# Kernel optimization log

Measured on AMD Instinct MI355X. Metric: run time of the kernel, lower is better.

## Reference

```python
import jax, jax.numpy as jnp
import numpy as np
from jax import lax

GAMMA = 1.0
BIG = 1e8  # matches the torch init value 100000000.0


def setup_inputs() -> dict:
    key = jax.random.key(0)
    k1, k2 = jax.random.split(key)
    B, n, m, d = 256, 256, 256, 32
    x = jax.random.normal(k1, (B, n, d), dtype=jnp.float32)
    y = jax.random.normal(k2, (B, m, d), dtype=jnp.float32)
    return {"x": x, "y": y}


def _soft_dtw(x, y, gamma):
    B, n, d = x.shape
    m = y.shape[1]
    # squared euclidean distances, (B, n, m); GEMM form avoids the (B,n,m,d) blowup
    x2 = jnp.sum(x * x, axis=-1)
    y2 = jnp.sum(y * y, axis=-1)
    dist = x2[:, :, None] + y2[:, None, :] - 2.0 * jnp.einsum('bnd,bmd->bnm', x, y)
    dist = jnp.maximum(dist, 0.0)  # cdist(p=2)**2 is nonnegative

    def softmin3(a, b, c):
        s = jnp.stack([a, b, c], axis=0)
        return -gamma * jax.nn.logsumexp(-s / gamma, axis=0)

    big_col = jnp.full((B,), BIG, dtype=x.dtype)

    def row_step(prev_row, d_row):
        # prev_row: (B, m+1) = D[i-1, :];  d_row: (B, m) = dist[:, i-1, :]
        def col_step(cur, inp):
            # cur: (B,) = D[i, j-1]; inp: (dist[i-1,j-1], D[i-1,j], D[i-1,j-1])
            dij, up, diag = inp
            new = dij + softmin3(up, cur, diag)
            return new, new
        xs = (d_row.T, prev_row[:, 1:].T, prev_row[:, :-1].T)  # each (m, B)
        _, vals = lax.scan(col_step, big_col, xs)  # vals: (m, B)
        new_row = jnp.concatenate([big_col[:, None], vals.T], axis=1)  # (B, m+1)
        return new_row, None

    init_row = jnp.concatenate(
        [jnp.zeros((B, 1), x.dtype), jnp.full((B, m), BIG, dtype=x.dtype)], axis=1)
    final_row, _ = lax.scan(row_step, init_row, jnp.swapaxes(dist, 0, 1))  # scan over n rows
    return jnp.mean(final_row[:, m])


def reference(x, y):
    return _soft_dtw(x, y, GAMMA)
```

## Files before the change

kernel.cpp:

```cpp
#include <hip/hip_runtime.h>

#define BIG 1e8f
#define LN2 0.69314718f
#define LOG2E 1.44269504f
#define M2L -2.8853900818f

#define RSLOT 112
#define DRB 1040

#define OFF_XH   116480
#define OFF_X2S  132864
#define OFF_Y2S  133888
#define OFF_RDY  134912
#define OFF_PRG  134976
#define LDS_BYTES 135040

typedef _Float16 half8 __attribute__((ext_vector_type(8)));
typedef _Float16 half2_t __attribute__((ext_vector_type(2)));
typedef float f32x4 __attribute__((ext_vector_type(4)));

__device__ __forceinline__ float exp2g(float x) {
#if __has_builtin(__builtin_amdgcn_exp2f)
    return __builtin_amdgcn_exp2f(x);
#else
    return exp2f(x);
#endif
}
__device__ __forceinline__ float log2g(float x) {
#if __has_builtin(__builtin_amdgcn_logf)
    return __builtin_amdgcn_logf(x);
#else
    return log2f(x);
#endif
}

__device__ __forceinline__ half2_t pkrtz(float a, float b) {
    return __builtin_bit_cast(half2_t, __builtin_amdgcn_cvt_pkrtz(a, b));
}

__device__ __forceinline__ float shfl_up1(float v, float oldv) {
    int r = __builtin_amdgcn_update_dpp(
        __builtin_bit_cast(int, oldv), __builtin_bit_cast(int, v),
        0x138 , 0xf, 0xf, false);
    return __builtin_bit_cast(float, r);
}

__device__ __forceinline__ void dec2(unsigned int w, float& a, float& b) {
    half2_t h = __builtin_bit_cast(half2_t, w);
    a = (float)h[0];
    b = (float)h[1];
}

#define MASKW0 0x7BFF7BFFu
#define MASKW1 0x70007000u
#define MASKW2 0x60006000u
#define MASKW3 0x50005000u

__global__ __launch_bounds__(128, 1) void sdtw_kernel(
    const float* __restrict__ x, const float* __restrict__ y,
    float* __restrict__ out) {
    extern __shared__ __align__(16) char smem[];
    unsigned char* band = (unsigned char*)smem;
    _Float16* xh = (_Float16*)(smem + OFF_XH);
    float* x2sL = (float*)(smem + OFF_X2S);
    float* y2sL = (float*)(smem + OFF_Y2S);
    volatile int* rdy = (volatile int*)(smem + OFF_RDY);
    volatile int* prg = (volatile int*)(smem + OFF_PRG);

    const int tid = threadIdx.x;
    const int b = blockIdx.x;
    const float* xb = x + (size_t)b * 8192;
    const float* yb = y + (size_t)b * 8192;

#pragma unroll
    for (int rr = 0; rr < 2; rr++) {
        const int r = tid + rr * 128;
        const float4* px = (const float4*)(xb + r * 32);
        union { _Float16 h[32]; half8 v[4]; } uc;
        float s2 = 0.f;
#pragma unroll
        for (int q = 0; q < 8; q++) {
            float4 f = px[q];
            s2 += f.x * f.x + f.y * f.y + f.z * f.z + f.w * f.w;
            uc.h[4 * q + 0] = (_Float16)f.x;
            uc.h[4 * q + 1] = (_Float16)f.y;
            uc.h[4 * q + 2] = (_Float16)f.z;
            uc.h[4 * q + 3] = (_Float16)f.w;
        }
        half8* dst = (half8*)&xh[r * 32];
#pragma unroll
        for (int q = 0; q < 4; q++) dst[q] = uc.v[q];
        x2sL[r] = s2 * LOG2E;

        const float4* py = (const float4*)(yb + r * 32);
        float t2 = 0.f;
#pragma unroll
        for (int q = 0; q < 8; q++) {
            float4 f = py[q];
            t2 += f.x * f.x + f.y * f.y + f.z * f.z + f.w * f.w;
        }
        y2sL[r] = t2 * LOG2E;
    }
    if (tid < 16) rdy[tid] = 0;
    if (tid == 16) *prg = 0;
    __syncthreads();

    if (tid >= 64) {
        const int lane = tid - 64;
        const int qd = lane >> 4, xr = lane & 15;

        half8 yfrag[16];
        float yvL[16];
#pragma unroll
        for (int ci = 0; ci < 16; ci++) {
            const float* yp = yb + (ci * 16 + xr) * 32 + qd * 8;
            float4 f0 = *(const float4*)yp;
            float4 f1 = *(const float4*)(yp + 4);
            half8 v;
            v[0] = (_Float16)f0.x; v[1] = (_Float16)f0.y;
            v[2] = (_Float16)f0.z; v[3] = (_Float16)f0.w;
            v[4] = (_Float16)f1.x; v[5] = (_Float16)f1.y;
            v[6] = (_Float16)f1.z; v[7] = (_Float16)f1.w;
            yfrag[ci] = v;
            yvL[ci] = y2sL[ci * 16 + xr];
        }

        for (int sg = 0; sg < 16; sg++) {
            if (sg >= 6) {
                const int need = 8 * sg - 40;
                while (*prg < need) {}
            }
            const half8 xf = *(const half8*)&xh[(sg * 16 + xr) * 32 + qd * 8];
            const float4 xl = *(const float4*)&x2sL[sg * 16 + qd * 4];
            const int p0 = 8 * sg + 2 * qd;
#pragma unroll
            for (int ci = 0; ci < 16; ci++) {
                f32x4 acc = {0.f, 0.f, 0.f, 0.f};
                acc = __builtin_amdgcn_mfma_f32_16x16x32_f16(xf, yfrag[ci], acc, 0, 0, 0);
                const int c = ci * 16 + xr;
                const float yv = yvL[ci];
                const float d0 = fmaxf(fmaf(M2L, acc[0], xl.x + yv), 0.f);
                const float d1 = fmaxf(fmaf(M2L, acc[1], xl.y + yv), 0.f);
                const float d2 = fmaxf(fmaf(M2L, acc[2], xl.z + yv), 0.f);
                const float d3 = fmaxf(fmaf(M2L, acc[3], xl.w + yv), 0.f);
                const half2_t h01 = pkrtz(d0, d1);
                const half2_t h23 = pkrtz(d2, d3);
                const int dr0 = p0 + (c >> 2);
                int s0_ = dr0;     if (s0_ >= RSLOT) s0_ -= RSLOT;
                int s1_ = dr0 + 1; if (s1_ >= RSLOT) s1_ -= RSLOT;
                *(half2_t*)&band[s0_ * DRB + 4 * c] = h01;
                *(half2_t*)&band[s1_ * DRB + 4 * c] = h23;
            }
            __threadfence_block();
            if (lane == 0) rdy[sg] = 1;
        }
        return;
    }

    const int lane = tid;
    float MpA3 = BIG, SpA3 = 1.f, MpB3 = BIG, SpB3 = 1.f;
    float Mm[4], Sm[4];
    Mm[0] = (lane == 0) ? 0.f : BIG;
    Sm[0] = (lane == 0) ? 1.f : 2.f;
    Mm[1] = BIG; Sm[1] = 2.f;
    Mm[2] = BIG; Sm[2] = 2.f;
    Mm[3] = BIG; Sm[3] = 2.f;

    while (rdy[0] == 0) {}
    uint4 wreg = *(const uint4*)&band[16 * lane];

    auto step = [&](int s_) {
        const float MLA = shfl_up1(MpA3, BIG);
        const float MLB = shfl_up1(MpB3, BIG);
        const float SLA = shfl_up1(SpA3, 1.f);
        const float SLB = shfl_up1(SpB3, 1.f);

        const bool act = (unsigned)(s_ - lane - 1) < 128u;
        const unsigned wx = act ? wreg.x : MASKW0;
        const unsigned wy = act ? wreg.y : MASKW1;
        const unsigned wz = act ? wreg.z : MASKW2;
        const unsigned ww = act ? wreg.w : MASKW3;
        float dA[4], dB[4];
        dec2(wx, dA[0], dB[0]);
        dec2(wy, dA[1], dB[1]);
        dec2(wz, dA[2], dB[2]);
        dec2(ww, dA[3], dB[3]);

        int dn = (s_ > 190) ? 190 : s_;
        if (dn >= RSLOT) dn -= RSLOT;
        const uint4 wnext = *(const uint4*)&band[dn * DRB + 16 * lane];

        float MA[4], xAm[4], xAv[4];
        float prevA = MLA;
#pragma unroll
        for (int k = 0; k < 4; k++) {
            const float mu = fminf(Mm[k], prevA);
            xAm[k] = mu - Mm[k];
            xAv[k] = mu - prevA;
            MA[k] = dA[k] + mu;
            prevA = MA[k];
        }
        float muN[4], xNa[4], xNb[4];
        float diagA = MLA;
#pragma unroll
        for (int k = 0; k < 4; k++) {
            muN[k] = fminf(MA[k], diagA);
            xNa[k] = muN[k] - MA[k];
            xNb[k] = muN[k] - diagA;
            diagA = MA[k];
        }
        float MB[4], xBm[4], xBv[4];
        float prevB = MLB;
#pragma unroll
        for (int k = 0; k < 4; k++) {
            const float mu = fminf(muN[k], prevB);
            xBm[k] = mu - muN[k];
            xBv[k] = mu - prevB;
            MB[k] = dB[k] + mu;
            prevB = MB[k];
        }
        float muC[4], xCa[4], xCb[4];
        float diagB = MLB;
#pragma unroll
        for (int k = 0; k < 4; k++) {
            muC[k] = fminf(MB[k], diagB);
            xCa[k] = muC[k] - MB[k];
            xCb[k] = muC[k] - diagB;
            diagB = MB[k];
        }

        float eAm[4], eAv[4], eNa[4], eNb[4], eBm[4], eBv[4], eCa[4], eCb[4];
#pragma unroll
        for (int k = 0; k < 4; k++) {
            eAm[k] = exp2g(xAm[k]);
            eAv[k] = exp2g(xAv[k]);
            eNa[k] = exp2g(xNa[k]);
            eNb[k] = exp2g(xNb[k]);
            eBm[k] = exp2g(xBm[k]);
            eBv[k] = exp2g(xBv[k]);
            eCa[k] = exp2g(xCa[k]);
            eCb[k] = exp2g(xCb[k]);
        }

        float SA[4];
        float ps = SLA;
#pragma unroll
        for (int k = 0; k < 4; k++) {
            SA[k] = fmaf(Sm[k], eAm[k], ps * eAv[k]);
            ps = SA[k];
        }
        float SN[4];
        float dsg = SLA;
#pragma unroll
        for (int k = 0; k < 4; k++) {
            SN[k] = fmaf(SA[k], eNa[k], dsg * eNb[k]);
            dsg = SA[k];
        }
        float SB[4];
        ps = SLB;
#pragma unroll
        for (int k = 0; k < 4; k++) {
            SB[k] = fmaf(SN[k], eBm[k], ps * eBv[k]);
            ps = SB[k];
        }
        dsg = SLB;
#pragma unroll
        for (int k = 0; k < 4; k++) {
            Sm[k] = fmaf(SB[k], eCa[k], dsg * eCb[k]);
            dsg = SB[k];
        }

        MpA3 = MA[3]; SpA3 = SA[3];
        MpB3 = MB[3]; SpB3 = SB[3];
#pragma unroll
        for (int k = 0; k < 4; k++) Mm[k] = muC[k];
        wreg = wnext;
    };

#pragma unroll
    for (int s_ = 1; s_ < 8; s_++) step(s_);

    for (int g = 1; g < 24; g++) {
        int st = (g > 15) ? 15 : g;
        while (rdy[st] == 0) {}
        if (lane == 0) *prg = 8 * g;
        const int s0 = 8 * g;
#pragma unroll
        for (int k = 0; k < 8; k++) step(s0 + k);
    }

    if (lane == 63)
        atomicAdd(out, (MpB3 - log2g(SpB3)) * (LN2 / 256.f));
}

extern "C" void kernel_launch(void* const* d_in, const int* in_sizes, int n_in,
                              void* d_out, int out_size, void* d_ws, size_t ws_size,
                              hipStream_t stream) {
    const float* x = (const float*)d_in[0];
    const float* y = (const float*)d_in[1];
    float* out = (float*)d_out;
    const int B = in_sizes[0] / (256 * 32);

    (void)hipFuncSetAttribute((const void*)sdtw_kernel,
                              hipFuncAttributeMaxDynamicSharedMemorySize,
                              LDS_BYTES);
    (void)hipMemsetAsync(d_out, 0, sizeof(float), stream);
    sdtw_kernel<<<dim3(B), dim3(128), LDS_BYTES, stream>>>(x, y, out);
}
```

Baseline: 134.8 us.

## Split soft-DTW wavefront into max-track and sum-track warps pipelined through LDS

Splits the single recurrence wave into two: one wave tracks the running minimum (M) and writes the per-step exponent gaps to an 8-deep LDS ring, and a second wave consumes them to update the scaled sums (S). The exp2 work also drops from two calls per softmin pair to one, using a sign-select on the gap. The block grows to 192 threads with a third wave for distance MFMA. The band ring shrinks to make room for the gap buffer, and the producer lookahead is adjusted. This adds LDS traffic and spin-wait handshakes between waves in exchange for shortening the serial dependency chain on each wave.

New measurement: 130.3 us. 3.4% less time.

```diff
diff --git a/kernel.cpp b/kernel.cpp
--- a/kernel.cpp
+++ b/kernel.cpp
@@ -5,15 +5,20 @@
 #define LOG2E 1.44269504f
 #define M2L -2.8853900818f
 
-#define RSLOT 112
+#define RSLOT 104
 #define DRB 1040
 
-#define OFF_XH   116480
-#define OFF_X2S  132864
-#define OFF_Y2S  133888
-#define OFF_RDY  134912
-#define OFF_PRG  134976
-#define LDS_BYTES 135040
+#define OFF_XH    108160
+#define OFF_X2S   124544
+#define OFF_Y2S   125568
+#define OFF_DR    126592
+#define OFF_RDY   159360
+#define OFF_PRG   159424
+#define OFF_MPRG  159428
+#define OFF_SPRG  159432
+#define OFF_MDONE 159436
+#define OFF_MVAL  159440
+#define LDS_BYTES 159456
 
 typedef _Float16 half8 __attribute__((ext_vector_type(8)));
 typedef _Float16 half2_t __attribute__((ext_vector_type(2)));
@@ -56,7 +61,7 @@
 #define MASKW2 0x60006000u
 #define MASKW3 0x50005000u
 
-__global__ __launch_bounds__(128, 1) void sdtw_kernel(
+__global__ __launch_bounds__(192, 1) void sdtw_kernel(
     const float* __restrict__ x, const float* __restrict__ y,
     float* __restrict__ out) {
     extern __shared__ __align__(16) char smem[];
@@ -66,47 +71,56 @@
     float* y2sL = (float*)(smem + OFF_Y2S);
     volatile int* rdy = (volatile int*)(smem + OFF_RDY);
     volatile int* prg = (volatile int*)(smem + OFF_PRG);
+    volatile int* mprg = (volatile int*)(smem + OFF_MPRG);
+    volatile int* sprg = (volatile int*)(smem + OFF_SPRG);
+    volatile int* mdone = (volatile int*)(smem + OFF_MDONE);
+    volatile float* mval = (volatile float*)(smem + OFF_MVAL);
 
     const int tid = threadIdx.x;
     const int b = blockIdx.x;
     const float* xb = x + (size_t)b * 8192;
     const float* yb = y + (size_t)b * 8192;
 
-#pragma unroll
-    for (int rr = 0; rr < 2; rr++) {
-        const int r = tid + rr * 128;
-        const float4* px = (const float4*)(xb + r * 32);
-        union { _Float16 h[32]; half8 v[4]; } uc;
-        float s2 = 0.f;
-#pragma unroll
-        for (int q = 0; q < 8; q++) {
-            float4 f = px[q];
-            s2 += f.x * f.x + f.y * f.y + f.z * f.z + f.w * f.w;
-            uc.h[4 * q + 0] = (_Float16)f.x;
-            uc.h[4 * q + 1] = (_Float16)f.y;
-            uc.h[4 * q + 2] = (_Float16)f.z;
-            uc.h[4 * q + 3] = (_Float16)f.w;
-        }
-        half8* dst = (half8*)&xh[r * 32];
-#pragma unroll
-        for (int q = 0; q < 4; q++) dst[q] = uc.v[q];
-        x2sL[r] = s2 * LOG2E;
-
-        const float4* py = (const float4*)(yb + r * 32);
-        float t2 = 0.f;
-#pragma unroll
-        for (int q = 0; q < 8; q++) {
-            float4 f = py[q];
-            t2 += f.x * f.x + f.y * f.y + f.z * f.z + f.w * f.w;
-        }
-        y2sL[r] = t2 * LOG2E;
+    if (tid < 128) {
+#pragma unroll
+        for (int rr = 0; rr < 2; rr++) {
+            const int r = tid + rr * 128;
+            const float4* px = (const float4*)(xb + r * 32);
+            union { _Float16 h[32]; half8 v[4]; } uc;
+            float s2 = 0.f;
+#pragma unroll
+            for (int q = 0; q < 8; q++) {
+                float4 f = px[q];
+                s2 += f.x * f.x + f.y * f.y + f.z * f.z + f.w * f.w;
+                uc.h[4 * q + 0] = (_Float16)f.x;
+                uc.h[4 * q + 1] = (_Float16)f.y;
+                uc.h[4 * q + 2] = (_Float16)f.z;
+                uc.h[4 * q + 3] = (_Float16)f.w;
+            }
+            half8* dst = (half8*)&xh[r * 32];
+#pragma unroll
+            for (int q = 0; q < 4; q++) dst[q] = uc.v[q];
+            x2sL[r] = s2 * LOG2E;
+
+            const float4* py = (const float4*)(yb + r * 32);
+            float t2 = 0.f;
+#pragma unroll
+            for (int q = 0; q < 8; q++) {
+                float4 f = py[q];
+                t2 += f.x * f.x + f.y * f.y + f.z * f.z + f.w * f.w;
+            }
+            y2sL[r] = t2 * LOG2E;
+        }
     }
     if (tid < 16) rdy[tid] = 0;
     if (tid == 16) *prg = 0;
+    if (tid == 17) *mprg = 0;
+    if (tid == 18) *sprg = 0;
+    if (tid == 19) *mdone = 0;
     __syncthreads();
 
-    if (tid >= 64) {
-        const int lane = tid - 64;
+    if (tid >= 128) {
+        const int lane = tid - 128;
         const int qd = lane >> 4, xr = lane & 15;
 
         half8 yfrag[16];
@@ -126,8 +140,8 @@
         }
 
         for (int sg = 0; sg < 16; sg++) {
-            if (sg >= 6) {
-                const int need = 8 * sg - 40;
+            if (sg >= 5) {
+                const int need = 8 * sg - 32;
                 while (*prg < need) {}
             }
             const half8 xf = *(const half8*)&xh[(sg * 16 + xr) * 32 + qd * 8];
@@ -157,140 +171,179 @@
         return;
     }
 
-    const int lane = tid;
-    float MpA3 = BIG, SpA3 = 1.f, MpB3 = BIG, SpB3 = 1.f;
-    float Mm[4], Sm[4];
-    Mm[0] = (lane == 0) ? 0.f : BIG;
-    Sm[0] = (lane == 0) ? 1.f : 2.f;
-    Mm[1] = BIG; Sm[1] = 2.f;
-    Mm[2] = BIG; Sm[2] = 2.f;
-    Mm[3] = BIG; Sm[3] = 2.f;
-
-    while (rdy[0] == 0) {}
-    uint4 wreg = *(const uint4*)&band[16 * lane];
-
-    auto step = [&](int s_) {
-        const float MLA = shfl_up1(MpA3, BIG);
-        const float MLB = shfl_up1(MpB3, BIG);
-        const float SLA = shfl_up1(SpA3, 1.f);
-        const float SLB = shfl_up1(SpB3, 1.f);
-
-        const bool act = (unsigned)(s_ - lane - 1) < 128u;
-        const unsigned wx = act ? wreg.x : MASKW0;
-        const unsigned wy = act ? wreg.y : MASKW1;
-        const unsigned wz = act ? wreg.z : MASKW2;
-        const unsigned ww = act ? wreg.w : MASKW3;
-        float dA[4], dB[4];
-        dec2(wx, dA[0], dB[0]);
-        dec2(wy, dA[1], dB[1]);
-        dec2(wz, dA[2], dB[2]);
-        dec2(ww, dA[3], dB[3]);
-
-        int dn = (s_ > 190) ? 190 : s_;
-        if (dn >= RSLOT) dn -= RSLOT;
-        const uint4 wnext = *(const uint4*)&band[dn * DRB + 16 * lane];
-
-        float MA[4], xAm[4], xAv[4];
-        float prevA = MLA;
-#pragma unroll
-        for (int k = 0; k < 4; k++) {
-            const float mu = fminf(Mm[k], prevA);
-            xAm[k] = mu - Mm[k];
-            xAv[k] = mu - prevA;
-            MA[k] = dA[k] + mu;
-            prevA = MA[k];
-        }
-        float muN[4], xNa[4], xNb[4];
-        float diagA = MLA;
-#pragma unroll
-        for (int k = 0; k < 4; k++) {
-            muN[k] = fminf(MA[k], diagA);
-            xNa[k] = muN[k] - MA[k];
-            xNb[k] = muN[k] - diagA;
-            diagA = MA[k];
-        }
-        float MB[4], xBm[4], xBv[4];
-        float prevB = MLB;
-#pragma unroll
-        for (int k = 0; k < 4; k++) {
-            const float mu = fminf(muN[k], prevB);
-            xBm[k] = mu - muN[k];
-            xBv[k] = mu - prevB;
-            MB[k] = dB[k] + mu;
-            prevB = MB[k];
-        }
-        float muC[4], xCa[4], xCb[4];
-        float diagB = MLB;
-#pragma unroll
-        for (int k = 0; k < 4; k++) {
-            muC[k] = fminf(MB[k], diagB);
-            xCa[k] = muC[k] - MB[k];
-            xCb[k] = muC[k] - diagB;
-            diagB = MB[k];
-        }
-
-        float eAm[4], eAv[4], eNa[4], eNb[4], eBm[4], eBv[4], eCa[4], eCb[4];
-#pragma unroll
-        for (int k = 0; k < 4; k++) {
-            eAm[k] = exp2g(xAm[k]);
-            eAv[k] = exp2g(xAv[k]);
-            eNa[k] = exp2g(xNa[k]);
-            eNb[k] = exp2g(xNb[k]);
-            eBm[k] = exp2g(xBm[k]);
-            eBv[k] = exp2g(xBv[k]);
-            eCa[k] = exp2g(xCa[k]);
-            eCb[k] = exp2g(xCb[k]);
-        }
-
-        float SA[4];
-        float ps = SLA;
-#pragma unroll
-        for (int k = 0; k < 4; k++) {
-            SA[k] = fmaf(Sm[k], eAm[k], ps * eAv[k]);
-            ps = SA[k];
-        }
-        float SN[4];
-        float dsg = SLA;
-#pragma unroll
-        for (int k = 0; k < 4; k++) {
-            SN[k] = fmaf(SA[k], eNa[k], dsg * eNb[k]);
-            dsg = SA[k];
-        }
-        float SB[4];
-        ps = SLB;
-#pragma unroll
-        for (int k = 0; k < 4; k++) {
-            SB[k] = fmaf(SN[k], eBm[k], ps * eBv[k]);
-            ps = SB[k];
-        }
-        dsg = SLB;
-#pragma unroll
-        for (int k = 0; k < 4; k++) {
-            Sm[k] = fmaf(SB[k], eCa[k], dsg * eCb[k]);
-            dsg = SB[k];
-        }
-
-        MpA3 = MA[3]; SpA3 = SA[3];
-        MpB3 = MB[3]; SpB3 = SB[3];
-#pragma unroll
-        for (int k = 0; k < 4; k++) Mm[k] = muC[k];
-        wreg = wnext;
-    };
-
-#pragma unroll
-    for (int s_ = 1; s_ < 8; s_++) step(s_);
-
-    for (int g = 1; g < 24; g++) {
-        int st = (g > 15) ? 15 : g;
-        while (rdy[st] == 0) {}
-        if (lane == 0) *prg = 8 * g;
-        const int s0 = 8 * g;
-#pragma unroll
-        for (int k = 0; k < 8; k++) step(s0 + k);
+    if (tid < 64) {
+        const int lane = tid;
+        float MpA3 = BIG, MpB3 = BIG;
+        float Mm[4];
+        Mm[0] = (lane == 0) ? 0.f : BIG;
+        Mm[1] = BIG; Mm[2] = BIG; Mm[3] = BIG;
+        char* dbase = (char*)smem + OFF_DR + lane * 16;
+
+        while (rdy[0] == 0) {}
+        uint4 wreg = *(const uint4*)&band[16 * lane];
+
+        auto mstep = [&](int s_) {
+            const float MLA = shfl_up1(MpA3, BIG);
+            const float MLB = shfl_up1(MpB3, BIG);
+
+            const bool act = (unsigned)(s_ - lane - 1) < 128u;
+            const unsigned wx = act ? wreg.x : MASKW0;
+            const unsigned wy = act ? wreg.y : MASKW1;
+            const unsigned wz = act ? wreg.z : MASKW2;
+            const unsigned ww = act ? wreg.w : MASKW3;
+            float dA[4], dB[4];
+            dec2(wx, dA[0], dB[0]);
+            dec2(wy, dA[1], dB[1]);
+            dec2(wz, dA[2], dB[2]);
+            dec2(ww, dA[3], dB[3]);
+
+            int dn = (s_ > 190) ? 190 : s_;
+            if (dn >= RSLOT) dn -= RSLOT;
+            const uint4 wnext = *(const uint4*)&band[dn * DRB + 16 * lane];
+
+            f32x4 gA, gN, gB, gC;
+            float MA[4];
+            float prevA = MLA;
+#pragma unroll
+            for (int k = 0; k < 4; k++) {
+                gA[k] = Mm[k] - prevA;
+                const float mu = fminf(Mm[k], prevA);
+                MA[k] = dA[k] + mu;
+                prevA = MA[k];
+            }
+            float muN[4];
+            float diagA = MLA;
+#pragma unroll
+            for (int k = 0; k < 4; k++) {
+                gN[k] = MA[k] - diagA;
+                muN[k] = fminf(MA[k], diagA);
+                diagA = MA[k];
+            }
+            float MB[4];
+            float prevB = MLB;
+#pragma unroll
+            for (int k = 0; k < 4; k++) {
+                gB[k] = muN[k] - prevB;
+                const float mu = fminf(muN[k], prevB);
+                MB[k] = dB[k] + mu;
+                prevB = MB[k];
+            }
+            float diagB = MLB;
+#pragma unroll
+            for (int k = 0; k < 4; k++) {
+                gC[k] = MB[k] - diagB;
+                Mm[k] = fminf(MB[k], diagB);
+                diagB = MB[k];
+            }
+
+            char* dp = dbase + (s_ & 7) * 4096;
+            *(f32x4*)(dp)        = gA;
+            *(f32x4*)(dp + 1024) = gN;
+            *(f32x4*)(dp + 2048) = gB;
+            *(f32x4*)(dp + 3072) = gC;
+
+            MpA3 = MA[3]; MpB3 = MB[3];
+            wreg = wnext;
+        };
+
+        auto mpair = [&](int s_) {
+            while (*sprg < s_ - 7) {}
+            mstep(s_); mstep(s_ + 1);
+            __threadfence_block();
+            if (lane == 0) *mprg = s_ + 1;
+        };
+
+        mstep(1);
+        __threadfence_block();
+        if (lane == 0) *mprg = 1;
+        mpair(2); mpair(4); mpair(6);
+
+        for (int g = 1; g < 24; g++) {
+            int st = (g > 15) ? 15 : g;
+            while (rdy[st] == 0) {}
+            if (lane == 0) *prg = 8 * g;
+            const int s0 = 8 * g;
+            mpair(s0); mpair(s0 + 2); mpair(s0 + 4); mpair(s0 + 6);
+        }
+
+        if (lane == 63) *mval = MpB3;
+        __threadfence_block();
+        if (lane == 0) *mdone = 1;
+        return;
     }
 
-    if (lane == 63)
-        atomicAdd(out, (MpB3 - log2g(SpB3)) * (LN2 / 256.f));
+    {
+        const int lane = tid - 64;
+        float SpA3 = 1.f, SpB3 = 1.f;
+        float Sm[4];
+        Sm[0] = (lane == 0) ? 1.f : 2.f;
+        Sm[1] = 2.f; Sm[2] = 2.f; Sm[3] = 2.f;
+        const char* dbase = (const char*)smem + OFF_DR + lane * 16;
+
+        while (*mprg < 3) {}
+        f32x4 cA = *(const f32x4*)(dbase + (1 & 7) * 4096);
+        f32x4 cN = *(const f32x4*)(dbase + (1 & 7) * 4096 + 1024);
+        f32x4 cB = *(const f32x4*)(dbase + (1 & 7) * 4096 + 2048);
+        f32x4 cC = *(const f32x4*)(dbase + (1 & 7) * 4096 + 3072);
+
+        auto sstep = [&](int s_) {
+            const int sn = (s_ >= 191) ? 191 : s_ + 1;
+            const char* np = dbase + (sn & 7) * 4096;
+            const f32x4 nA = *(const f32x4*)(np);
+            const f32x4 nN = *(const f32x4*)(np + 1024);
+            const f32x4 nB = *(const f32x4*)(np + 2048);
+            const f32x4 nC = *(const f32x4*)(np + 3072);
+
+            const float SLA = shfl_up1(SpA3, 1.f);
+            const float SLB = shfl_up1(SpB3, 1.f);
+
+            float SA[4];
+            float ps = SLA;
+#pragma unroll
+            for (int k = 0; k < 4; k++) {
+                const float e = exp2g(-fabsf(cA[k]));
+                SA[k] = (cA[k] <= 0.f) ? fmaf(ps, e, Sm[k]) : fmaf(Sm[k], e, ps);
+                ps = SA[k];
+            }
+            float SN[4];
+            float dsg = SLA;
+#pragma unroll
+            for (int k = 0; k < 4; k++) {
+                const float e = exp2g(-fabsf(cN[k]));
+                SN[k] = (cN[k] <= 0.f) ? fmaf(dsg, e, SA[k]) : fmaf(SA[k], e, dsg);
+                dsg = SA[k];
+            }
+            float SB[4];
+            ps = SLB;
+#pragma unroll
+            for (int k = 0; k < 4; k++) {
+                const float e = exp2g(-fabsf(cB[k]));
+                SB[k] = (cB[k] <= 0.f) ? fmaf(ps, e, SN[k]) : fmaf(SN[k], e, ps);
+                ps = SB[k];
+            }
+            dsg = SLB;
+#pragma unroll
+            for (int k = 0; k < 4; k++) {
+                const float e = exp2g(-fabsf(cC[k]));
+                Sm[k] = (cC[k] <= 0.f) ? fmaf(dsg, e, SB[k]) : fmaf(SB[k], e, dsg);
+                dsg = SB[k];
+            }
+            SpA3 = SA[3]; SpB3 = SB[3];
+            cA = nA; cN = nN; cB = nB; cC = nC;
+        };
+
+        for (int u0 = 1; u0 <= 189; u0 += 2) {
+            while (*mprg < u0 + 2) {}
+            sstep(u0); sstep(u0 + 1);
+            if (lane == 0) *sprg = u0 + 1;
+        }
+        while (*mprg < 191) {}
+        sstep(191);
+
+        while (*mdone == 0) {}
+        if (lane == 63)
+            atomicAdd(out, ((*mval) - log2g(SpB3)) * (LN2 / 256.f));
+    }
 }
 
 extern "C" void kernel_launch(void* const* d_in, const int* in_sizes, int n_in,
@@ -305,5 +358,5 @@
                               hipFuncAttributeMaxDynamicSharedMemorySize,
                               LDS_BYTES);
     (void)hipMemsetAsync(d_out, 0, sizeof(float), stream);
-    sdtw_kernel<<<dim3(B), dim3(128), LDS_BYTES, stream>>>(x, y, out);
-}
+    sdtw_kernel<<<dim3(B), dim3(192), LDS_BYTES, stream>>>(x, y, out);
+}
```
